# Optimization experiments

Hardware: AMD Instinct MI355X
Metric: run time of the kernel (lower is better)

The kernel has to match this reference:

```python
import jax, jax.numpy as jnp
import numpy as np
from jax import lax

B, H, W = 2, 512, 512
K = 200                 # TOP_K_INSTANCE: fixed candidate-center budget (jit-static)
SIGMA = 8
RAD = 3 * SIGMA + 1     # Gaussian half-window (25); window = [c-RAD, c+RAD]
THR = 0.1               # POST_PROCESSING.CENTER_THRESHOLD
THR_CENTER = 0.1        # cfg.THRESHOLD_CENTER
NMS_K = 7               # POST_PROCESSING.NMS_KERNEL
MIN_PXL = 64            # cfg.CENTER_PSEUDO_LBL_MIN_PXL
THING = jnp.array([11, 12, 13, 14, 15, 16, 17, 18], dtype=jnp.int32)
BIG = jnp.float32(1e10)


def setup_inputs() -> dict:
    key = jax.random.key(0)
    k1, k2, k3, k4 = jax.random.split(key, 4)
    ctr_hmp = jax.random.uniform(k1, (B, 1, H, W), dtype=jnp.float32)
    offsets = jax.random.normal(k2, (B, 2, H, W), dtype=jnp.float32) * 8.0
    semantic_pred = jax.random.randint(k3, (B, H, W), 0, 19, dtype=jnp.int32)
    mixmasks = (jax.random.uniform(k4, (B, 1, H, W)) < 0.3).astype(jnp.float32)
    return {"ctr_hmp": ctr_hmp, "offsets": offsets,
            "semantic_pred": semantic_pred, "mixmasks": mixmasks}


def reference(ctr_hmp, offsets, semantic_pred, mixmasks):
    # ---- _find_instance_center: threshold + maxpool NMS -> peak candidates ----
    hmp = jnp.where(ctr_hmp > THR, ctr_hmp, -1.0)                      # F.threshold
    pooled = lax.reduce_window(hmp, -jnp.inf, lax.max,
                               (1, 1, NMS_K, NMS_K), (1, 1, 1, 1), 'SAME')
    peaks = jnp.where(hmp == pooled, hmp, -1.0)[:, 0]                  # [B,H,W]
    vals, idx = lax.top_k(peaks.reshape(B * H * W), K)                 # fixed K candidates
    valid = vals >= THR_CENTER
    bids = idx // (H * W)
    cys = (idx % (H * W)) // W
    cxs = idx % W

    # ---- thing_seg_map ----
    thing = (semantic_pred[..., None] == THING).any(-1).astype(jnp.float32)  # [B,H,W]

    # ---- _gen_pseudo_labels: filter centers, Gaussian-splat with max ----
    valid &= mixmasks[bids, 0, cys, cxs] < 0.5                         # MixMask == 1 -> skip
    # window sum of thing_seg_map via integral image
    ii = jnp.pad(jnp.cumsum(jnp.cumsum(thing, axis=1), axis=2),
                 ((0, 0), (1, 0), (1, 0)))                             # [B,H+1,W+1]
    y0 = jnp.clip(cys - RAD, 0, H); y1 = jnp.clip(cys + RAD + 1, 0, H)
    x0 = jnp.clip(cxs - RAD, 0, W); x1 = jnp.clip(cxs + RAD + 1, 0, W)
    wsum = ii[bids, y1, x1] - ii[bids, y0, x1] - ii[bids, y1, x0] + ii[bids, y0, x0]
    selected = valid & (wsum >= MIN_PXL)                               # [K]

    yy = jnp.arange(H, dtype=jnp.float32)
    xx = jnp.arange(W, dtype=jnp.float32)
    dy = yy[None, :] - cys[:, None].astype(jnp.float32)                # [K,H]
    dx = xx[None, :] - cxs[:, None].astype(jnp.float32)                # [K,W]
    inv2s2 = 1.0 / (2.0 * SIGMA * SIGMA)
    gy = jnp.exp(-dy * dy * inv2s2) * (jnp.abs(dy) <= RAD)             # separable Gaussian
    gx = jnp.exp(-dx * dx * inv2s2) * (jnp.abs(dx) <= RAD)
    contrib = gy[:, :, None] * gx[:, None, :]                          # [K,H,W]
    seg_ids = jnp.where(selected, bids, B)                             # invalid -> dump slot
    center = jax.ops.segment_max(contrib, seg_ids, num_segments=B + 1)[:B]
    center = jnp.maximum(center, 0.0)[:, None]                         # [B,1,H,W]

    # ---- _group_pixels_without_for_loop: nearest-center argmin ----
    coord = jnp.stack(jnp.meshgrid(yy, xx, indexing='ij'), axis=0)     # [2,H,W] (y,x)
    ctr_loc = (coord[None] + offsets).transpose(0, 2, 3, 1).reshape(B, H * W, 2)
    c = jnp.stack([cys, cxs], axis=1).astype(jnp.float32)              # [K,2]
    d2 = (jnp.sum(c * c, axis=1)[:, None, None]
          - 2.0 * jnp.einsum('kc,bnc->kbn', c, ctr_loc)
          + jnp.sum(ctr_loc * ctr_loc, axis=-1)[None])                 # [K,B,HW]
    in_batch = selected[:, None] & (bids[:, None] == jnp.arange(B)[None, :])  # [K,B]
    d2m = jnp.where(in_batch[:, :, None], d2, BIG)
    amin = jnp.argmin(d2m, axis=0)                                     # [B,HW] global k
    # per-batch local index (original returns index within the batch's own center list)
    kk = jnp.arange(K)
    prior = (kk[None, :] < kk[:, None]) & (bids[None, :] == bids[:, None]) & selected[None, :]
    local_idx = prior.sum(axis=1)                                      # [K]
    any_center = in_batch.any(axis=0)                                  # [B]
    seg_id = jnp.where(any_center[:, None], local_idx[amin] + 1, 0)    # [B,HW]
    ins = thing * seg_id.reshape(B, H, W).astype(jnp.float32)          # [B,H,W]

    # ---- offset pseudo labels: per-instance mass-center minus pixel coord ----
    ins_int = ins.astype(jnp.int32)                                    # 0..K
    segg = (jnp.arange(B, dtype=jnp.int32)[:, None, None] * (K + 1) + ins_int).reshape(-1)
    nseg = B * (K + 1)
    ycf = jnp.broadcast_to(coord[0], (B, H, W)).reshape(-1)
    xcf = jnp.broadcast_to(coord[1], (B, H, W)).reshape(-1)
    cnt = jax.ops.segment_sum(jnp.ones_like(ycf), segg, num_segments=nseg)
    my = jax.ops.segment_sum(ycf, segg, num_segments=nseg) / jnp.maximum(cnt, 1.0)
    mx = jax.ops.segment_sum(xcf, segg, num_segments=nseg) / jnp.maximum(cnt, 1.0)
    fg = ins > 0
    off_y = jnp.where(fg, my[segg].reshape(B, H, W) - coord[0][None], 0.0)
    off_x = jnp.where(fg, mx[segg].reshape(B, H, W) - coord[1][None], 0.0)
    offset_pseudo_label = jnp.stack([off_y, off_x], axis=1)            # [B,2,H,W]

    center_weights = jnp.ones((B, H, W), dtype=jnp.int32)
    offset_weights = fg.astype(jnp.int32)
    return center, offset_pseudo_label, center_weights, offset_weights
```

## Files before the change

kernel.cpp:

```cpp
#include <hip/hip_runtime.h>

constexpr int B_ = 2, H_ = 512, W_ = 512;
constexpr int HWl = H_ * W_;
constexpr int TOT = B_ * HWl;
constexpr int KC = 200;
constexpr int NBLK = 256;
constexpr int BINOFF = 0x3DCCC;
constexpr float INV2S2 = 0.0078125f;

constexpr int OUT_CENTER = 0;
constexpr int OUT_OFF = TOT;
constexpr int OUT_CW = 3 * TOT;
constexpr int OUT_OW = 4 * TOT;

__device__ __forceinline__ float hwthr(float v) { return v > 0.1f ? v : -1.0f; }
__device__ __forceinline__ float4 max4(float4 a, float4 b) {
  return make_float4(fmaxf(a.x, b.x), fmaxf(a.y, b.y), fmaxf(a.z, b.z), fmaxf(a.w, b.w));
}
__device__ __forceinline__ int finebin(unsigned long long kk) {
  int bq = (int)(kk >> 44) - BINOFF;
  return bq < 0 ? 0 : (bq > 8191 ? 8191 : bq);
}


__global__ __launch_bounds__(256) void k_nms(const float* __restrict__ ctr,
                                             unsigned long long* __restrict__ keys,
                                             int* __restrict__ bcount) {
  __shared__ float rmx[10 * 512];
  __shared__ unsigned long long lkeys[1024];
  __shared__ int lnum;
  int tid = threadIdx.x, blk = blockIdx.x;
  int b = blk >> 7, y0 = (blk & 127) << 2;
  if (tid == 0) lnum = 0;
  const float4* c4p = (const float4*)(ctr + b * HWl);
  for (int u = tid; u < 1280; u += 256) {
    int r = u >> 7, c4 = u & 127, gy = y0 - 3 + r;
    float4 m = make_float4(-1e30f, -1e30f, -1e30f, -1e30f);
    if (gy >= 0 && gy < H_) {
      float4 v = c4p[gy * 128 + c4];
      float4 L = make_float4(-1e30f, -1e30f, -1e30f, -1e30f), R = L;
      if (c4 > 0) L = c4p[gy * 128 + c4 - 1];
      if (c4 < 127) R = c4p[gy * 128 + c4 + 1];
      float a1 = hwthr(L.y), a2 = hwthr(L.z), a3 = hwthr(L.w);
      float a4 = hwthr(v.x), a5 = hwthr(v.y), a6 = hwthr(v.z), a7 = hwthr(v.w);
      float a8 = hwthr(R.x), a9 = hwthr(R.y), a10 = hwthr(R.z);
      float core = fmaxf(fmaxf(a4, a5), fmaxf(a6, a7));
      m.x = fmaxf(fmaxf(a1, a2), fmaxf(a3, core));
      m.y = fmaxf(fmaxf(a2, a3), fmaxf(core, a8));
      m.z = fmaxf(fmaxf(a3, core), fmaxf(a8, a9));
      m.w = fmaxf(fmaxf(core, a8), fmaxf(a9, a10));
    }
    ((float4*)rmx)[u] = m;
  }
  __syncthreads();
  for (int u = tid; u < 512; u += 256) {
    int orr = u >> 7, c4 = u & 127;
    int y = y0 + orr;
    float4 pool = ((float4*)rmx)[orr * 128 + c4];
#pragma unroll
    for (int r = 1; r <= 6; ++r)
      pool = max4(pool, ((float4*)rmx)[(orr + r) * 128 + c4]);
    float4 v = c4p[y * 128 + c4];
    float vv[4] = {v.x, v.y, v.z, v.w};
    float pv[4] = {pool.x, pool.y, pool.z, pool.w};
#pragma unroll
    for (int j = 0; j < 4; ++j) {
      float vj = vv[j];
      if (vj > 0.1f && vj == pv[j]) {
        unsigned int i = (unsigned int)(b * HWl + y * W_ + c4 * 4 + j);
        unsigned long long comp = ((unsigned long long)__float_as_uint(vj) << 32)
                                | (unsigned long long)(0xFFFFFFFFu - i);
        int slot = atomicAdd(&lnum, 1);
        if (slot < 1024) lkeys[slot] = comp;
      }
    }
  }
  __syncthreads();
  int n = lnum; if (n > 1024) n = 1024;
  if (tid == 0) bcount[blk] = n;
  for (int q = tid; q < n; q += 256) keys[blk * 1024 + q] = lkeys[q];
}

__global__ __launch_bounds__(1024) void k_sel(
    const unsigned long long* __restrict__ keys, const int* __restrict__ bcount,
    float* __restrict__ cand_val, int* __restrict__ cand_bid,
    int* __restrict__ cand_cy, int* __restrict__ cand_cx) {
  __shared__ int hist[8192];
  __shared__ int sfx[1024];
  __shared__ int bc[NBLK];
  __shared__ int s_P1, ln;
  __shared__ unsigned long long wk[1024];
  int tid = threadIdx.x;
  if (tid == 0) { s_P1 = 0; ln = 0; }
  if (tid < NBLK) { int c = bcount[tid]; bc[tid] = c > 1024 ? 1024 : c; }
  for (int q = tid; q < 8192; q += 1024) hist[q] = 0;
  __syncthreads();
  int seg = tid >> 2, sub = tid & 3;
  int nn = bc[seg];
  for (int q = sub; q < nn; q += 4)
    atomicAdd(&hist[finebin(keys[seg * 1024 + q])], 1);
  __syncthreads();
  int bins[8];
  int cs = 0;
#pragma unroll
  for (int q = 0; q < 8; ++q) { bins[q] = hist[tid * 8 + q]; cs += bins[q]; }
  sfx[tid] = cs;
  __syncthreads();
  for (int off = 1; off < 1024; off <<= 1) {
    int v = (tid + off < 1024) ? sfx[tid + off] : 0;
    __syncthreads();
    sfx[tid] += v;
    __syncthreads();
  }
  int total = sfx[0];
  if (total > KC) {
    int above = (tid == 1023) ? 0 : sfx[tid + 1];
    if (sfx[tid] >= KC && above < KC) {
      int acc = above;
#pragma unroll
      for (int bq = 7; bq >= 0; --bq) {
        acc += bins[bq];
        if (acc >= KC) { s_P1 = tid * 8 + bq; break; }
      }
    }
  }
  __syncthreads();
  int P1 = s_P1;
  for (int q = sub; q < nn; q += 4) {
    unsigned long long kk = keys[seg * 1024 + q];
    if (finebin(kk) >= P1) {
      int w2 = atomicAdd(&ln, 1);
      if (w2 < 1024) wk[w2] = kk;
    }
  }
  __syncthreads();
  int n = ln > 1024 ? 1024 : ln;
  if (tid < n) {
    unsigned long long mine = wk[tid];
    int r = 0;
    for (int j = 0; j < n; ++j) r += (wk[j] > mine) ? 1 : 0;
    if (r < KC) {
      unsigned int key32 = (unsigned int)(mine >> 32);
      unsigned int idx = 0xFFFFFFFFu - (unsigned int)(mine & 0xFFFFFFFFULL);
      int bb = (int)(idx >> 18), rem = (int)(idx & (HWl - 1));
      cand_val[r] = __uint_as_float(key32);
      cand_bid[r] = bb; cand_cy[r] = rem >> 9; cand_cx[r] = rem & (W_ - 1);
    }
  }
  if (tid >= n && tid < KC) {
    cand_val[tid] = -1e30f; cand_bid[tid] = 0; cand_cy[tid] = 0; cand_cx[tid] = 0;
  }
}

__global__ __launch_bounds__(256) void k_wsum(
    const int* __restrict__ sem, const float* __restrict__ mix,
    const float* __restrict__ cand_val, const int* __restrict__ cand_bid,
    const int* __restrict__ cand_cy, const int* __restrict__ cand_cx,
    int* __restrict__ selected, int* __restrict__ gz) {
  __shared__ int ssum[256];
  if (blockIdx.x == 0) {
    for (int q = threadIdx.x; q < 3 * (KC + 1) * B_; q += 256) gz[q] = 0;
  }
  int k = blockIdx.x;
  int b = cand_bid[k], cy = cand_cy[k], cx = cand_cx[k];
  float v = cand_val[k];
  int y0 = cy - 25; if (y0 < 0) y0 = 0;
  int y1 = cy + 26; if (y1 > H_) y1 = H_;
  int x0 = cx - 25; if (x0 < 0) x0 = 0;
  int x1 = cx + 26; if (x1 > W_) x1 = W_;
  int wd = x1 - x0, nr = y1 - y0;
  int wave = threadIdx.x >> 6, lane = threadIdx.x & 63;
  int s = 0;
  for (int rr = wave; rr < nr; rr += 4) {
    if (lane < wd) {
      int sv = sem[b * HWl + (y0 + rr) * W_ + x0 + lane];
      s += (sv >= 11 && sv <= 18) ? 1 : 0;
    }
  }
  ssum[threadIdx.x] = s;
  __syncthreads();
  for (int o = 128; o > 0; o >>= 1) {
    if (threadIdx.x < o) ssum[threadIdx.x] += ssum[threadIdx.x + o];
    __syncthreads();
  }
  if (threadIdx.x == 0) {
    bool sel = (v >= 0.1f) && (mix[b * HWl + cy * W_ + cx] < 0.5f) && (ssum[0] >= 64);
    selected[k] = sel ? 1 : 0;
  }
}

__global__ __launch_bounds__(256) void k_fused(
    const float* __restrict__ offs, const int* __restrict__ sem,
    const int* __restrict__ cand_bid, const int* __restrict__ cand_cy,
    const int* __restrict__ cand_cx, const int* __restrict__ selected,
    int* __restrict__ ins, float* __restrict__ out,
    int* __restrict__ gsy, int* __restrict__ gsx, int* __restrict__ gcn) {
  __shared__ float4 sc[KC];
  __shared__ float2 gl[KC];
  __shared__ int lsy[KC + 1], lsx[KC + 1], lcn[KC + 1];
  __shared__ int wtot[4];
  __shared__ int gcnt_s;
  int tid = threadIdx.x;
  int t = blockIdx.x * 256 + tid;
  int p = t << 2;
  int b = p >> 18;
  int rem = p & (HWl - 1), y = rem >> 9, x0i = rem & (W_ - 1);
  int yA = (int)(((unsigned)(blockIdx.x * 1024) & (HWl - 1)) >> 9);

  for (int q = tid; q <= KC; q += 256) { lsy[q] = 0; lsx[q] = 0; lcn[q] = 0; }
  if (tid == 0) gcnt_s = 0;
  bool sel = false; int cb = 0, ccy = 0, ccx = 0;
  if (tid < KC) { sel = selected[tid] != 0; cb = cand_bid[tid]; ccy = cand_cy[tid]; ccx = cand_cx[tid]; }
  bool mine = sel && (cb == b);
  unsigned long long mk = __ballot(mine);
  int lane = tid & 63, wv = tid >> 6;
  if (lane == 0) wtot[wv] = __popcll(mk);
  __syncthreads();
  int base = 0;
  for (int w2 = 0; w2 < wv; ++w2) base += wtot[w2];
  int S = wtot[0] + wtot[1] + wtot[2] + wtot[3];
  if (mine) {
    int pos = base + __popcll(mk & ((1ULL << lane) - 1ULL));
    float fyc = (float)ccy, fxc = (float)ccx;
    float cc = __fadd_rn(__fmul_rn(fyc, fyc), __fmul_rn(fxc, fxc));
    sc[pos] = make_float4(fyc, fxc, cc, 0.0f);
  }
  __syncthreads();
  if (tid < S) {
    float cyv = sc[tid].x;
    if (cyv >= (float)(yA - 25) && cyv <= (float)(yA + 26)) {
      int gp = atomicAdd(&gcnt_s, 1);
      gl[gp] = make_float2(cyv, sc[tid].y);
    }
  }
  __syncthreads();
  int G = gcnt_s;

  float fy = (float)y;
  float4 oy4 = *(const float4*)(offs + b * 2 * HWl + rem);
  float4 ox4 = *(const float4*)(offs + b * 2 * HWl + HWl + rem);
  float oyv[4] = {oy4.x, oy4.y, oy4.z, oy4.w};
  float oxv[4] = {ox4.x, ox4.y, ox4.z, ox4.w};
  float lyv[4], lxv[4], llv[4], bd[4];
  int bsg[4];
#pragma unroll
  for (int j = 0; j < 4; ++j) {
    float fx = (float)(x0i + j);
    lyv[j] = __fadd_rn(fy, oyv[j]);
    lxv[j] = __fadd_rn(fx, oxv[j]);
    llv[j] = __fadd_rn(__fmul_rn(lyv[j], lyv[j]), __fmul_rn(lxv[j], lxv[j]));
    bd[j] = 3.0e38f; bsg[j] = 0;
  }
  for (int s = 0; s < S; ++s) {
    float4 c = sc[s];
#pragma unroll
    for (int j = 0; j < 4; ++j) {
      float dot = __fadd_rn(__fmul_rn(c.x, lyv[j]), __fmul_rn(c.y, lxv[j]));
      float d2 = __fadd_rn(__fsub_rn(c.z, __fmul_rn(2.0f, dot)), llv[j]);
      bool better = d2 < bd[j];
      bd[j] = better ? d2 : bd[j];
      bsg[j] = better ? (s + 1) : bsg[j];
    }
  }
  float bg[4] = {0.0f, 0.0f, 0.0f, 0.0f};
  for (int g = 0; g < G; ++g) {
    float2 gc = gl[g];
    float dyc = fy - gc.x;
    if (fabsf(dyc) <= 25.0f) {
      float gy = expf(-__fmul_rn(__fmul_rn(dyc, dyc), INV2S2));
#pragma unroll
      for (int j = 0; j < 4; ++j) {
        float dxc = (float)(x0i + j) - gc.y;
        if (fabsf(dxc) <= 25.0f) {
          float gx = expf(-__fmul_rn(__fmul_rn(dxc, dxc), INV2S2));
          bg[j] = fmaxf(bg[j], __fmul_rn(gy, gx));
        }
      }
    }
  }
  *(float4*)(out + OUT_CENTER + p) = make_float4(bg[0], bg[1], bg[2], bg[3]);
  int4 sv4 = *(const int4*)(sem + p);
  int svv[4] = {sv4.x, sv4.y, sv4.z, sv4.w};
  int insv[4];
  bool s_any = S > 0;
#pragma unroll
  for (int j = 0; j < 4; ++j) {
    bool thing = (svv[j] >= 11 && svv[j] <= 18);
    insv[j] = (thing && s_any) ? bsg[j] : 0;
  }
  *(int4*)(ins + p) = make_int4(insv[0], insv[1], insv[2], insv[3]);
  int curSeg = -1, aY = 0, aX = 0, aC = 0;
#pragma unroll
  for (int j = 0; j < 4; ++j) {
    if (insv[j] > 0) {
      int sg = insv[j];
      if (sg != curSeg) {
        if (curSeg >= 0) {
          atomicAdd(&lsy[curSeg], aY); atomicAdd(&lsx[curSeg], aX); atomicAdd(&lcn[curSeg], aC);
        }
        curSeg = sg; aY = 0; aX = 0; aC = 0;
      }
      aY += y; aX += x0i + j; aC += 1;
    }
  }
  if (curSeg >= 0) {
    atomicAdd(&lsy[curSeg], aY); atomicAdd(&lsx[curSeg], aX); atomicAdd(&lcn[curSeg], aC);
  }
  __syncthreads();
  for (int q = tid; q <= KC; q += 256) {
    int c = lcn[q];
    if (c) {
      int gq = b * (KC + 1) + q;
      atomicAdd(&gcn[gq], c); atomicAdd(&gsy[gq], lsy[q]); atomicAdd(&gsx[gq], lsx[q]);
    }
  }
}

__global__ __launch_bounds__(256) void k_off(
    const int* __restrict__ ins, const int* __restrict__ gsy,
    const int* __restrict__ gsx, const int* __restrict__ gcn,
    float* __restrict__ out) {
  int t = blockIdx.x * 256 + threadIdx.x;
  int p = t << 2;
  int b = p >> 18, rem = p & (HWl - 1), y = rem >> 9, x0i = rem & (W_ - 1);
  int4 iv = *(const int4*)(ins + p);
  int insv[4] = {iv.x, iv.y, iv.z, iv.w};
  float oy[4], ox[4], ow[4];
  float fy = (float)y;
#pragma unroll
  for (int j = 0; j < 4; ++j) {
    if (insv[j] > 0) {
      int sg = b * (KC + 1) + insv[j];
      float c = fmaxf((float)gcn[sg], 1.0f);
      oy[j] = __fsub_rn((float)gsy[sg] / c, fy);
      ox[j] = __fsub_rn((float)gsx[sg] / c, (float)(x0i + j));
      ow[j] = 1.0f;
    } else { oy[j] = 0.0f; ox[j] = 0.0f; ow[j] = 0.0f; }
  }
  *(float4*)(out + OUT_OFF + b * 2 * HWl + rem) = make_float4(oy[0], oy[1], oy[2], oy[3]);
  *(float4*)(out + OUT_OFF + b * 2 * HWl + HWl + rem) = make_float4(ox[0], ox[1], ox[2], ox[3]);
  *(float4*)(out + OUT_CW + p) = make_float4(1.0f, 1.0f, 1.0f, 1.0f);
  *(float4*)(out + OUT_OW + p) = make_float4(ow[0], ow[1], ow[2], ow[3]);
}

extern "C" void kernel_launch(void* const* d_in, const int* in_sizes, int n_in,
                              void* d_out, int out_size, void* d_ws, size_t ws_size,
                              hipStream_t stream) {
  const float* ctr = (const float*)d_in[0];
  const float* offs = (const float*)d_in[1];
  const int* sem = (const int*)d_in[2];
  const float* mix = (const float*)d_in[3];
  float* out = (float*)d_out;

  char* w = (char*)d_ws;
  int* gz = (int*)(w + 0);
  int* gsy = gz;
  int* gsx = gz + (KC + 1) * B_;
  int* gcn = gz + 2 * (KC + 1) * B_;
  int* bcount = (int*)(w + 8192);
  float* cand_val = (float*)(w + 10240);
  int* cand_bid = (int*)(w + 11264);
  int* cand_cy = (int*)(w + 12288);
  int* cand_cx = (int*)(w + 13312);
  int* selected = (int*)(w + 14336);
  unsigned long long* keys = (unsigned long long*)(w + 65536);
  int* ins = (int*)(w + 65536);

  k_nms<<<NBLK, 256, 0, stream>>>(ctr, keys, bcount);
  k_sel<<<1, 1024, 0, stream>>>(keys, bcount,
                                cand_val, cand_bid, cand_cy, cand_cx);
  k_wsum<<<KC, 256, 0, stream>>>(sem, mix, cand_val, cand_bid, cand_cy, cand_cx,
                                 selected, gz);
  k_fused<<<512, 256, 0, stream>>>(offs, sem, cand_bid, cand_cy, cand_cx, selected,
                                   ins, out, gsy, gsx, gcn);
  k_off<<<512, 256, 0, stream>>>(ins, gsy, gsx, gcn, out);
}
```

Baseline: 51.75 us.

## Merge window-sum, splat and offset kernels into one grid-barrier persistent kernel

Fuses the candidate window-sum, Gaussian splat/segment-accumulation, and offset-label kernels into a single 512-block kernel. A hand-written atomic grid barrier separates the phases, and the barrier counters are reset in k_sel. The per-pixel instance map is now kept in registers across the barrier instead of going through a global buffer. This aims to cut kernel launch gaps and the ins round-trip through memory. In exchange it depends on all 512 blocks being co-resident (launch bounds of 2 blocks per CU) and adds spin-wait barrier latency.

```diff
diff --git a/kernel.cpp b/kernel.cpp
--- a/kernel.cpp
+++ b/kernel.cpp
@@ -5,6 +5,7 @@
 constexpr int TOT = B_ * HWl;
 constexpr int KC = 200;
 constexpr int NBLK = 256;
+constexpr int GRID = 512;
 constexpr int BINOFF = 0x3DCCC;
 constexpr float INV2S2 = 0.0078125f;
 
@@ -20,6 +21,18 @@
 __device__ __forceinline__ int finebin(unsigned long long kk) {
   int bq = (int)(kk >> 44) - BINOFF;
   return bq < 0 ? 0 : (bq > 8191 ? 8191 : bq);
+}
+
+__device__ __forceinline__ void gridbar(int* cnt, int target) {
+  __threadfence();
+  __syncthreads();
+  if (threadIdx.x == 0) {
+    __hip_atomic_fetch_add(cnt, 1, __ATOMIC_ACQ_REL, __HIP_MEMORY_SCOPE_AGENT);
+    while (__hip_atomic_load(cnt, __ATOMIC_ACQUIRE, __HIP_MEMORY_SCOPE_AGENT) < target) {
+      __builtin_amdgcn_s_sleep(8);
+    }
+  }
+  __syncthreads();
 }
 
 
@@ -84,7 +97,8 @@
 __global__ __launch_bounds__(1024) void k_sel(
     const unsigned long long* __restrict__ keys, const int* __restrict__ bcount,
     float* __restrict__ cand_val, int* __restrict__ cand_bid,
-    int* __restrict__ cand_cy, int* __restrict__ cand_cx) {
+    int* __restrict__ cand_cy, int* __restrict__ cand_cx,
+    int* __restrict__ barcnt) {
   __shared__ int hist[8192];
   __shared__ int sfx[1024];
   __shared__ int bc[NBLK];
@@ -92,6 +106,7 @@
   __shared__ unsigned long long wk[1024];
   int tid = threadIdx.x;
   if (tid == 0) { s_P1 = 0; ln = 0; }
+  if (tid < 2) barcnt[tid] = 0;
   if (tid < NBLK) { int c = bcount[tid]; bc[tid] = c > 1024 ? 1024 : c; }
   for (int q = tid; q < 8192; q += 1024) hist[q] = 0;
   __syncthreads();
@@ -152,65 +167,68 @@
   }
 }
 
-__global__ __launch_bounds__(256) void k_wsum(
-    const int* __restrict__ sem, const float* __restrict__ mix,
+__global__ __launch_bounds__(256, 2) void k_mega(
+    const float* __restrict__ offs, const int* __restrict__ sem,
+    const float* __restrict__ mix,
     const float* __restrict__ cand_val, const int* __restrict__ cand_bid,
     const int* __restrict__ cand_cy, const int* __restrict__ cand_cx,
-    int* __restrict__ selected, int* __restrict__ gz) {
-  __shared__ int ssum[256];
-  if (blockIdx.x == 0) {
-    for (int q = threadIdx.x; q < 3 * (KC + 1) * B_; q += 256) gz[q] = 0;
-  }
-  int k = blockIdx.x;
-  int b = cand_bid[k], cy = cand_cy[k], cx = cand_cx[k];
-  float v = cand_val[k];
-  int y0 = cy - 25; if (y0 < 0) y0 = 0;
-  int y1 = cy + 26; if (y1 > H_) y1 = H_;
-  int x0 = cx - 25; if (x0 < 0) x0 = 0;
-  int x1 = cx + 26; if (x1 > W_) x1 = W_;
-  int wd = x1 - x0, nr = y1 - y0;
-  int wave = threadIdx.x >> 6, lane = threadIdx.x & 63;
-  int s = 0;
-  for (int rr = wave; rr < nr; rr += 4) {
-    if (lane < wd) {
-      int sv = sem[b * HWl + (y0 + rr) * W_ + x0 + lane];
-      s += (sv >= 11 && sv <= 18) ? 1 : 0;
-    }
-  }
-  ssum[threadIdx.x] = s;
-  __syncthreads();
-  for (int o = 128; o > 0; o >>= 1) {
-    if (threadIdx.x < o) ssum[threadIdx.x] += ssum[threadIdx.x + o];
-    __syncthreads();
-  }
-  if (threadIdx.x == 0) {
-    bool sel = (v >= 0.1f) && (mix[b * HWl + cy * W_ + cx] < 0.5f) && (ssum[0] >= 64);
-    selected[k] = sel ? 1 : 0;
-  }
-}
-
-__global__ __launch_bounds__(256) void k_fused(
-    const float* __restrict__ offs, const int* __restrict__ sem,
-    const int* __restrict__ cand_bid, const int* __restrict__ cand_cy,
-    const int* __restrict__ cand_cx, const int* __restrict__ selected,
-    int* __restrict__ ins, float* __restrict__ out,
-    int* __restrict__ gsy, int* __restrict__ gsx, int* __restrict__ gcn) {
+    int* __restrict__ selected,
+    int* __restrict__ gsy, int* __restrict__ gsx, int* __restrict__ gcn,
+    int* __restrict__ barcnt, float* __restrict__ out) {
   __shared__ float4 sc[KC];
   __shared__ float2 gl[KC];
   __shared__ int lsy[KC + 1], lsx[KC + 1], lcn[KC + 1];
+  __shared__ int ssum[256];
   __shared__ int wtot[4];
   __shared__ int gcnt_s;
-  int tid = threadIdx.x;
-  int t = blockIdx.x * 256 + tid;
+  int tid = threadIdx.x, blk = blockIdx.x;
+
+  if (blk == 0) {
+    for (int q = tid; q < 3 * (KC + 1) * B_; q += 256) gsy[q] = 0;
+  }
+  if (blk < KC) {
+    int k = blk;
+    int cb = cand_bid[k], cy = cand_cy[k], cx = cand_cx[k];
+    float v = cand_val[k];
+    int wy0 = cy - 25; if (wy0 < 0) wy0 = 0;
+    int wy1 = cy + 26; if (wy1 > H_) wy1 = H_;
+    int wx0 = cx - 25; if (wx0 < 0) wx0 = 0;
+    int wx1 = cx + 26; if (wx1 > W_) wx1 = W_;
+    int wd = wx1 - wx0, nr = wy1 - wy0;
+    int wave = tid >> 6, lane = tid & 63;
+    int s = 0;
+    for (int rr = wave; rr < nr; rr += 4) {
+      if (lane < wd) {
+        int sv = sem[cb * HWl + (wy0 + rr) * W_ + wx0 + lane];
+        s += (sv >= 11 && sv <= 18) ? 1 : 0;
+      }
+    }
+    ssum[tid] = s;
+    __syncthreads();
+    for (int o = 128; o > 0; o >>= 1) {
+      if (tid < o) ssum[tid] += ssum[tid + o];
+      __syncthreads();
+    }
+    if (tid == 0) {
+      bool sel = (v >= 0.1f) && (mix[cb * HWl + cy * W_ + cx] < 0.5f) && (ssum[0] >= 64);
+      selected[k] = sel ? 1 : 0;
+    }
+  }
+  gridbar(barcnt + 0, GRID);
+
+  int t = blk * 256 + tid;
   int p = t << 2;
   int b = p >> 18;
   int rem = p & (HWl - 1), y = rem >> 9, x0i = rem & (W_ - 1);
-  int yA = (int)(((unsigned)(blockIdx.x * 1024) & (HWl - 1)) >> 9);
+  int yA = (int)(((unsigned)(blk * 1024) & (HWl - 1)) >> 9);
 
   for (int q = tid; q <= KC; q += 256) { lsy[q] = 0; lsx[q] = 0; lcn[q] = 0; }
   if (tid == 0) gcnt_s = 0;
   bool sel = false; int cb = 0, ccy = 0, ccx = 0;
-  if (tid < KC) { sel = selected[tid] != 0; cb = cand_bid[tid]; ccy = cand_cy[tid]; ccx = cand_cx[tid]; }
+  if (tid < KC) {
+    sel = __hip_atomic_load(&selected[tid], __ATOMIC_RELAXED, __HIP_MEMORY_SCOPE_AGENT) != 0;
+    cb = cand_bid[tid]; ccy = cand_cy[tid]; ccx = cand_cx[tid];
+  }
   bool mine = sel && (cb == b);
   unsigned long long mk = __ballot(mine);
   int lane = tid & 63, wv = tid >> 6;
@@ -288,7 +306,6 @@
     bool thing = (svv[j] >= 11 && svv[j] <= 18);
     insv[j] = (thing && s_any) ? bsg[j] : 0;
   }
-  *(int4*)(ins + p) = make_int4(insv[0], insv[1], insv[2], insv[3]);
   int curSeg = -1, aY = 0, aX = 0, aC = 0;
 #pragma unroll
   for (int j = 0; j < 4; ++j) {
@@ -314,26 +331,23 @@
       atomicAdd(&gcn[gq], c); atomicAdd(&gsy[gq], lsy[q]); atomicAdd(&gsx[gq], lsx[q]);
     }
   }
-}
-
-__global__ __launch_bounds__(256) void k_off(
-    const int* __restrict__ ins, const int* __restrict__ gsy,
-    const int* __restrict__ gsx, const int* __restrict__ gcn,
-    float* __restrict__ out) {
-  int t = blockIdx.x * 256 + threadIdx.x;
-  int p = t << 2;
-  int b = p >> 18, rem = p & (HWl - 1), y = rem >> 9, x0i = rem & (W_ - 1);
-  int4 iv = *(const int4*)(ins + p);
-  int insv[4] = {iv.x, iv.y, iv.z, iv.w};
+  gridbar(barcnt + 1, GRID);
+
+  for (int q = tid; q <= KC; q += 256) {
+    int gq = b * (KC + 1) + q;
+    lsy[q] = __hip_atomic_load(&gsy[gq], __ATOMIC_RELAXED, __HIP_MEMORY_SCOPE_AGENT);
+    lsx[q] = __hip_atomic_load(&gsx[gq], __ATOMIC_RELAXED, __HIP_MEMORY_SCOPE_AGENT);
+    lcn[q] = __hip_atomic_load(&gcn[gq], __ATOMIC_RELAXED, __HIP_MEMORY_SCOPE_AGENT);
+  }
+  __syncthreads();
   float oy[4], ox[4], ow[4];
-  float fy = (float)y;
 #pragma unroll
   for (int j = 0; j < 4; ++j) {
     if (insv[j] > 0) {
-      int sg = b * (KC + 1) + insv[j];
-      float c = fmaxf((float)gcn[sg], 1.0f);
-      oy[j] = __fsub_rn((float)gsy[sg] / c, fy);
-      ox[j] = __fsub_rn((float)gsx[sg] / c, (float)(x0i + j));
+      int sg = insv[j];
+      float c = fmaxf((float)lcn[sg], 1.0f);
+      oy[j] = __fsub_rn((float)lsy[sg] / c, fy);
+      ox[j] = __fsub_rn((float)lsx[sg] / c, (float)(x0i + j));
       ow[j] = 1.0f;
     } else { oy[j] = 0.0f; ox[j] = 0.0f; ow[j] = 0.0f; }
   }
@@ -357,6 +371,7 @@
   int* gsy = gz;
   int* gsx = gz + (KC + 1) * B_;
   int* gcn = gz + 2 * (KC + 1) * B_;
+  int* barcnt = (int*)(w + 5120);
   int* bcount = (int*)(w + 8192);
   float* cand_val = (float*)(w + 10240);
   int* cand_bid = (int*)(w + 11264);
@@ -364,14 +379,11 @@
   int* cand_cx = (int*)(w + 13312);
   int* selected = (int*)(w + 14336);
   unsigned long long* keys = (unsigned long long*)(w + 65536);
-  int* ins = (int*)(w + 65536);
 
   k_nms<<<NBLK, 256, 0, stream>>>(ctr, keys, bcount);
   k_sel<<<1, 1024, 0, stream>>>(keys, bcount,
-                                cand_val, cand_bid, cand_cy, cand_cx);
-  k_wsum<<<KC, 256, 0, stream>>>(sem, mix, cand_val, cand_bid, cand_cy, cand_cx,
-                                 selected, gz);
-  k_fused<<<512, 256, 0, stream>>>(offs, sem, cand_bid, cand_cy, cand_cx, selected,
-                                   ins, out, gsy, gsx, gcn);
-  k_off<<<512, 256, 0, stream>>>(ins, gsy, gsx, gcn, out);
-}
+                                cand_val, cand_bid, cand_cy, cand_cx, barcnt);
+  k_mega<<<GRID, 256, 0, stream>>>(offs, sem, mix,
+                                   cand_val, cand_bid, cand_cy, cand_cx, selected,
+                                   gsy, gsx, gcn, barcnt, out);
+}
```

After: 181.7 us. +251.0%, slower.
